# Performance work log

Hardware: AMD Instinct MI355X
Metric: run time of the kernel (lower is better)

The kernel has to match this reference:

```python
import jax, jax.numpy as jnp
import numpy as np

WINDOW_SIZE = (4, 7, 7)  # (t, h, w); N = 4*7*7 = 196


def _relative_position_index(ws):
    t, h, w = ws
    coords = np.stack(np.meshgrid(np.arange(t), np.arange(h), np.arange(w), indexing='ij'))  # (3,t,h,w)
    cf = coords.reshape(3, -1)                      # (3, N)
    rc = (cf[:, :, None] - cf[:, None, :]).transpose(1, 2, 0).astype(np.int64)  # (N, N, 3)
    rc[..., 0] += t - 1
    rc[..., 1] += h - 1
    rc[..., 2] += w - 1
    rc[..., 0] *= (2 * h - 1) * (2 * w - 1)
    rc[..., 1] *= 2 * w - 1
    return rc.sum(-1)                               # (N, N) indices into bias table


def setup_inputs() -> dict:
    key = jax.random.key(0)
    ks = jax.random.split(key, 7)
    B, B_dim, N, C, H = 4, 64, 196, 512, 16
    hd = C // H
    B_ = B * B_dim
    n_bias = (2 * 4 - 1) * (2 * 7 - 1) * (2 * 7 - 1)  # 1183
    return {
        'x': jax.random.normal(ks[0], (B_, N, C), jnp.float32),
        'q_global': jax.random.normal(ks[1], (B, 1, H, N, hd), jnp.float32),
        'kv_w': jax.random.normal(ks[2], (2 * C, C), jnp.float32) * (C ** -0.5),
        'kv_b': jnp.zeros((2 * C,), jnp.float32),
        'proj_w': jax.random.normal(ks[3], (C, C), jnp.float32) * (C ** -0.5),
        'proj_b': jnp.zeros((C,), jnp.float32),
        'bias_table': jax.random.normal(ks[4], (n_bias, H), jnp.float32) * 0.02,
    }


def reference(x, q_global, kv_w, kv_b, proj_w, proj_b, bias_table):
    B_, N, C = x.shape
    B, _, H, _, hd = q_global.shape
    B_dim = B_ // B
    scale = hd ** -0.5

    # kv projection: (B_, N, 2C) -> k, v each (B_, H, N, hd)
    kv = (x @ kv_w.T + kv_b).reshape(B_, N, 2, H, hd).transpose(2, 0, 3, 1, 4)
    keys, values = kv[0], kv[1]

    # global queries repeated across windows: (B,1,H,N,hd) -> (B_, H, N, hd)
    q = jnp.broadcast_to(q_global, (B, B_dim, H, N, hd)).reshape(B_, H, N, hd)
    q = q * scale

    attn = jnp.einsum('bhnd,bhmd->bhnm', q, keys)  # (B_, H, N, N)

    # gathered relative position bias (static index table)
    rpi = jnp.asarray(_relative_position_index(WINDOW_SIZE))  # (N, N)
    bias = bias_table[rpi.reshape(-1)].reshape(N, N, H).transpose(2, 0, 1)  # (H, N, N)
    attn = jax.nn.softmax(attn + bias[None], axis=-1)

    out = jnp.einsum('bhnm,bhmd->bhnd', attn, values)  # (B_, H, N, hd)
    out = out.transpose(0, 2, 1, 3).reshape(B_, N, C)
    return out @ proj_w.T + proj_b
```

## Files before the change

kernel.cpp:

```cpp
#include <hip/hip_runtime.h>
#include <stdint.h>

typedef __attribute__((ext_vector_type(8))) short short8;
typedef __attribute__((ext_vector_type(4))) float f32x4;
typedef __attribute__((ext_vector_type(4))) unsigned short u16x4;

typedef unsigned short ushort_t;

__device__ __forceinline__ unsigned short f2bf(float f) {
    union { float f; uint32_t u; } c; c.f = f;
    uint32_t u = c.u;
    return (unsigned short)((u + 0x7FFFu + ((u >> 16) & 1u)) >> 16);
}

__device__ __forceinline__ f32x4 mfma16(short8 a, short8 b, f32x4 c) {
    return __builtin_amdgcn_mfma_f32_16x16x32_bf16(a, b, c, 0, 0, 0);
}

__device__ __forceinline__ void gl_lds16(const ushort_t* g, ushort_t* l) {
    __builtin_amdgcn_global_load_lds((const __attribute__((address_space(1))) void*)g,
                                     (__attribute__((address_space(3))) void*)l, 16, 0, 0);
}

#define LOG2E 1.4426950408889634f


__global__ __launch_bounds__(256) void cvt_x_k(const float4* __restrict__ in,
                                               u16x4* __restrict__ out, int n4) {
    int i = blockIdx.x * 256 + threadIdx.x;
    if (i < n4) {
        float4 v = in[i];
        u16x4 o;
        o[0] = f2bf(v.x); o[1] = f2bf(v.y); o[2] = f2bf(v.z); o[3] = f2bf(v.w);
        out[i] = o;
    }
}

__global__ __launch_bounds__(256) void cvt_small_k(const float4* __restrict__ kvw,
                                                   const float4* __restrict__ pw,
                                                   const float4* __restrict__ qg,
                                                   u16x4* __restrict__ kvwb,
                                                   u16x4* __restrict__ pwb,
                                                   u16x4* __restrict__ qb) {
    const float qs = 0.17677669529663687f * LOG2E;
    int i = blockIdx.x * 256 + threadIdx.x;
    if (i < 131072) {
        float4 v = kvw[i];
        u16x4 o; o[0]=f2bf(v.x); o[1]=f2bf(v.y); o[2]=f2bf(v.z); o[3]=f2bf(v.w);
        kvwb[i] = o;
    } else if (i < 196608) {
        int j = i - 131072;
        float4 v = pw[j];
        u16x4 o; o[0]=f2bf(v.x); o[1]=f2bf(v.y); o[2]=f2bf(v.z); o[3]=f2bf(v.w);
        pwb[j] = o;
    } else {
        int j = i - 196608;
        float4 v = qg[j];
        u16x4 o; o[0]=f2bf(v.x*qs); o[1]=f2bf(v.y*qs); o[2]=f2bf(v.z*qs); o[3]=f2bf(v.w*qs);
        qb[j] = o;
    }
}

__global__ __launch_bounds__(256) void bias_k(const float* __restrict__ bt,
                                              float* __restrict__ out) {
    int idx = blockIdx.x * 256 + threadIdx.x;
    int h = idx / 43264;
    int rem = idx - h * 43264;
    int i = rem / 208;
    int j = rem - i * 208;
    float v = -1e30f;
    if (i < 196 && j < 196) {
        int t1 = i / 49, r1 = i - t1 * 49, h1 = r1 / 7, w1 = r1 - h1 * 7;
        int t2 = j / 49, r2 = j - t2 * 49, h2 = r2 / 7, w2 = r2 - h2 * 7;
        int bi = (t1 - t2 + 3) * 169 + (h1 - h2 + 6) * 13 + (w1 - w2 + 6);
        v = bt[bi * 16 + h] * LOG2E;
    }
    out[idx] = v;
}

__global__ __launch_bounds__(256) void gemm_kv(const ushort_t* __restrict__ A,
                                               const ushort_t* __restrict__ Bw,
                                               const float* __restrict__ kvb,
                                               ushort_t* __restrict__ Ko,
                                               ushort_t* __restrict__ Vo) {
    __shared__ ushort_t As[128 * 64];
    __shared__ ushort_t Bs[128 * 64];
    const int tid = threadIdx.x;
    const int lane = tid & 63, wave = tid >> 6;
    const int lrow = lane & 15, quad = lane >> 4;
    const int wr = wave >> 1, wc = wave & 1;
    const long arow0 = (long)blockIdx.x * 128;
    const int brow0 = blockIdx.y * 128;

    const int srow = lane >> 3;
    const int scol = ((lane & 7) ^ srow) << 3;
    const int rsw  = (lrow & 7) << 3;

    f32x4 acc[4][4];
#pragma unroll
    for (int i = 0; i < 4; ++i)
#pragma unroll
        for (int j = 0; j < 4; ++j) acc[i][j] = (f32x4){0.f, 0.f, 0.f, 0.f};

    for (int k0 = 0; k0 < 512; k0 += 64) {
#pragma unroll
        for (int t = 0; t < 4; ++t) {
            int rr = wave * 32 + t * 8;
            gl_lds16(&A[(arow0 + rr + srow) * 512 + k0 + scol], &As[rr * 64]);
            gl_lds16(&Bw[(long)(brow0 + rr + srow) * 512 + k0 + scol], &Bs[rr * 64]);
        }
        asm volatile("s_waitcnt vmcnt(0)" ::: "memory");
        __syncthreads();
#pragma unroll
        for (int kk = 0; kk < 64; kk += 32) {
            short8 af[4], bf[4];
#pragma unroll
            for (int i = 0; i < 4; ++i)
                af[i] = *(const short8*)&As[(wr * 64 + i * 16 + lrow) * 64 + ((kk + quad * 8) ^ rsw)];
#pragma unroll
            for (int j = 0; j < 4; ++j)
                bf[j] = *(const short8*)&Bs[(wc * 64 + j * 16 + lrow) * 64 + ((kk + quad * 8) ^ rsw)];
#pragma unroll
            for (int i = 0; i < 4; ++i)
#pragma unroll
                for (int j = 0; j < 4; ++j)
                    acc[i][j] = mfma16(af[i], bf[j], acc[i][j]);
        }
        __syncthreads();
    }
#pragma unroll
    for (int i = 0; i < 4; ++i) {
        int mb = (int)arow0 + wr * 64 + i * 16 + quad * 4;
#pragma unroll
        for (int r = 0; r < 4; ++r) {
            int m = mb + r;
            int b_ = m / 196;
            int n = m - b_ * 196;
#pragma unroll
            for (int j = 0; j < 4; ++j) {
                int cI = brow0 + wc * 64 + j * 16 + lrow;
                float v = acc[i][j][r] + kvb[cI];
                int hh = (cI >> 5) & 15, d = cI & 31;
                ushort_t* dst = (cI >> 9) ? Vo : Ko;
                dst[((((long)b_ << 4) + hh) * 196 + n) * 32 + d] = f2bf(v);
            }
        }
    }
}

__global__ __launch_bounds__(256) void attn_k(const ushort_t* __restrict__ Kb,
                                              const ushort_t* __restrict__ Vb,
                                              const ushort_t* __restrict__ Qb,
                                              const float* __restrict__ biasF,
                                              ushort_t* __restrict__ Ob) {
    const int tid = threadIdx.x, lane = tid & 63, wave = tid >> 6;
    const int lrow = lane & 15, quad = lane >> 4;
    const int bh = blockIdx.x;
    const int b_ = bh >> 4, h = bh & 15;
    const int Bq = b_ >> 6;

    __shared__ ushort_t Vt[32 * 232];
    __shared__ ushort_t Ps[4][16 * 232];

    const long kvoff = (long)bh * 6272;

    for (int i = tid; i < 1024; i += 256) {
        int d = i >> 5, n = 192 + (i & 31);
        Vt[d * 232 + n] = 0;
    }
    __syncthreads();
    for (int i = tid; i < 6272; i += 256) {
        int n = i >> 5, d = i & 31;
        int g = (d >> 3) & 3;
        Vt[d * 232 + (n ^ (g << 3))] = Vb[kvoff + i];
    }
    for (int i = lane; i < 256; i += 64) {
        int r = i >> 4, cp = i & 15;
        Ps[wave][r * 232 + 208 + cp] = 0;
    }
    __syncthreads();

    const float* biasH = biasF + h * 43264;
    const long qbase = (((long)Bq * 16 + h) * 196) * 32;
    const ushort_t* Kh = Kb + kvoff;
    const int vsw0 = ((lrow >> 3) & 1) << 3;
    const int vsw1 = (2 | ((lrow >> 3) & 1)) << 3;

    for (int rt = wave; rt < 13; rt += 4) {
        const int qrow = rt * 16 + lrow;
        const int qr = qrow > 195 ? 195 : qrow;
        short8 qf = *(const short8*)&Qb[qbase + (long)qr * 32 + quad * 8];

        f32x4 s[13];
#pragma unroll
        for (int ct = 0; ct < 13; ++ct) {
            short8 kf = *(const short8*)&Kh[(ct * 16 + lrow) * 32 + quad * 8];
            s[ct] = mfma16(kf, qf, (f32x4){0.f, 0.f, 0.f, 0.f});
        }

        float mx = -3e38f;
        const float* bp = biasH + (long)qrow * 208 + quad * 4;
#pragma unroll
        for (int ct = 0; ct < 13; ++ct) {
            float4 bv = *(const float4*)&bp[ct * 16];
            s[ct][0] += bv.x; s[ct][1] += bv.y; s[ct][2] += bv.z; s[ct][3] += bv.w;
            mx = fmaxf(mx, fmaxf(fmaxf(s[ct][0], s[ct][1]), fmaxf(s[ct][2], s[ct][3])));
        }
        mx = fmaxf(mx, __shfl_xor(mx, 16));
        mx = fmaxf(mx, __shfl_xor(mx, 32));

        float sm = 0.f;
#pragma unroll
        for (int ct = 0; ct < 13; ++ct)
#pragma unroll
            for (int r = 0; r < 4; ++r) {
                float p = exp2f(s[ct][r] - mx);
                s[ct][r] = p;
                sm += p;
            }
        sm += __shfl_xor(sm, 16);
        sm += __shfl_xor(sm, 32);
        const float sminv = 1.0f / sm;

        ushort_t* prow = &Ps[wave][lrow * 232];
#pragma unroll
        for (int ct = 0; ct < 13; ++ct) {
            uint32_t w0, w1;
            asm("v_cvt_pk_bf16_f32 %0, %1, %2" : "=v"(w0) : "v"(s[ct][0]), "v"(s[ct][1]));
            asm("v_cvt_pk_bf16_f32 %0, %1, %2" : "=v"(w1) : "v"(s[ct][2]), "v"(s[ct][3]));
            uint2 w; w.x = w0; w.y = w1;
            *(uint2*)&prow[ct * 16 + quad * 4] = w;
        }
        asm volatile("s_waitcnt lgkmcnt(0)" ::: "memory");

        f32x4 o0 = (f32x4){0.f,0.f,0.f,0.f}, o1 = (f32x4){0.f,0.f,0.f,0.f};
#pragma unroll
        for (int ks = 0; ks < 7; ++ks) {
            short8 pf = *(const short8*)&prow[ks * 32 + quad * 8];
            short8 v0 = *(const short8*)&Vt[lrow * 232 + ((ks * 32 + quad * 8) ^ vsw0)];
            short8 v1 = *(const short8*)&Vt[(16 + lrow) * 232 + ((ks * 32 + quad * 8) ^ vsw1)];
            o0 = mfma16(pf, v0, o0);
            o1 = mfma16(pf, v1, o1);
        }
        const long obase = (long)b_ * 196 * 512 + h * 32;
#pragma unroll
        for (int r = 0; r < 4; ++r) {
            float sv = __shfl(sminv, quad * 4 + r);
            int m = rt * 16 + quad * 4 + r;
            if (m < 196) {
                Ob[obase + (long)m * 512 + lrow]      = f2bf(o0[r] * sv);
                Ob[obase + (long)m * 512 + 16 + lrow] = f2bf(o1[r] * sv);
            }
        }
    }
}

__global__ __launch_bounds__(256) void gemm_proj(const ushort_t* __restrict__ A,
                                                 const ushort_t* __restrict__ Bw,
                                                 const float* __restrict__ pb,
                                                 float* __restrict__ out) {
    __shared__ ushort_t As[128 * 64];
    __shared__ ushort_t Bs[128 * 64];
    const int tid = threadIdx.x;
    const int lane = tid & 63, wave = tid >> 6;
    const int lrow = lane & 15, quad = lane >> 4;
    const int wr = wave >> 1, wc = wave & 1;
    const long arow0 = (long)blockIdx.x * 128;
    const int brow0 = blockIdx.y * 128;

    const int srow = lane >> 3;
    const int scol = ((lane & 7) ^ srow) << 3;
    const int rsw  = (lrow & 7) << 3;

    f32x4 acc[4][4];
#pragma unroll
    for (int i = 0; i < 4; ++i)
#pragma unroll
        for (int j = 0; j < 4; ++j) acc[i][j] = (f32x4){0.f, 0.f, 0.f, 0.f};

    for (int k0 = 0; k0 < 512; k0 += 64) {
#pragma unroll
        for (int t = 0; t < 4; ++t) {
            int rr = wave * 32 + t * 8;
            gl_lds16(&A[(arow0 + rr + srow) * 512 + k0 + scol], &As[rr * 64]);
            gl_lds16(&Bw[(long)(brow0 + rr + srow) * 512 + k0 + scol], &Bs[rr * 64]);
        }
        asm volatile("s_waitcnt vmcnt(0)" ::: "memory");
        __syncthreads();
#pragma unroll
        for (int kk = 0; kk < 64; kk += 32) {
            short8 af[4], bf[4];
#pragma unroll
            for (int i = 0; i < 4; ++i)
                af[i] = *(const short8*)&As[(wr * 64 + i * 16 + lrow) * 64 + ((kk + quad * 8) ^ rsw)];
#pragma unroll
            for (int j = 0; j < 4; ++j)
                bf[j] = *(const short8*)&Bs[(wc * 64 + j * 16 + lrow) * 64 + ((kk + quad * 8) ^ rsw)];
#pragma unroll
            for (int i = 0; i < 4; ++i)
#pragma unroll
                for (int j = 0; j < 4; ++j)
                    acc[i][j] = mfma16(af[i], bf[j], acc[i][j]);
        }
        __syncthreads();
    }
#pragma unroll
    for (int i = 0; i < 4; ++i) {
        long mb = arow0 + wr * 64 + i * 16 + quad * 4;
#pragma unroll
        for (int r = 0; r < 4; ++r) {
            long m = mb + r;
#pragma unroll
            for (int j = 0; j < 4; ++j) {
                int cI = brow0 + wc * 64 + j * 16 + lrow;
                out[m * 512 + cI] = acc[i][j][r] + pb[cI];
            }
        }
    }
}


extern "C" void kernel_launch(void* const* d_in, const int* in_sizes, int n_in,
                              void* d_out, int out_size, void* d_ws, size_t ws_size,
                              hipStream_t stream) {
    const float* x   = (const float*)d_in[0];
    const float* qg  = (const float*)d_in[1];
    const float* kvw = (const float*)d_in[2];
    const float* kvb = (const float*)d_in[3];
    const float* pw  = (const float*)d_in[4];
    const float* pb  = (const float*)d_in[5];
    const float* bt  = (const float*)d_in[6];
    float* out = (float*)d_out;

    char* ws = (char*)d_ws;
    ushort_t* xb    = (ushort_t*)(ws);
    ushort_t* kbuf  = (ushort_t*)(ws + 51380224);
    ushort_t* vbuf  = (ushort_t*)(ws + 102760448);
    ushort_t* kvwb  = (ushort_t*)(ws + 154140672);
    ushort_t* pwb   = (ushort_t*)(ws + 155189248);
    ushort_t* qb    = (ushort_t*)(ws + 155713536);
    float*    biasF = (float*)   (ws + 156516352);
    ushort_t* obuf  = xb;

    cvt_x_k<<<25088, 256, 0, stream>>>((const float4*)x, (u16x4*)xb, 6422528);
    cvt_small_k<<<1160, 256, 0, stream>>>((const float4*)kvw, (const float4*)pw,
                                          (const float4*)qg,
                                          (u16x4*)kvwb, (u16x4*)pwb, (u16x4*)qb);
    bias_k<<<2704, 256, 0, stream>>>(bt, biasF);
    gemm_kv<<<dim3(392, 8), 256, 0, stream>>>(xb, kvwb, kvb, kbuf, vbuf);
    attn_k<<<4096, 256, 0, stream>>>(kbuf, vbuf, qb, biasF, obuf);
    gemm_proj<<<dim3(392, 4), 256, 0, stream>>>(obuf, pwb, pb, out);
}
```

Measured before the change: 446.0 us.

## Store V transposed from the KV GEMM and read it directly in attention

The KV projection epilogue now writes V in a transposed, padded layout (head-dim major, 200-wide token rows), packing four consecutive tokens per store. A small kernel zeroes the four padding columns of each row. The attention kernel no longer stages and transposes V through shared memory with scalar stores and barriers; it loads the B fragments for the P·V MMA straight from global memory. This removes the per-block LDS transpose and its barriers. In exchange, each wave rereads V from cache and the K and V output stores in the GEMM epilogue become more scattered.

```diff
diff --git a/kernel.cpp b/kernel.cpp
--- a/kernel.cpp
+++ b/kernel.cpp
@@ -61,6 +61,12 @@
     }
 }
 
+__global__ __launch_bounds__(256) void zeroT_k(ushort_t* __restrict__ vt) {
+    int i = blockIdx.x * 256 + threadIdx.x;
+    u16x4 z = (u16x4){0, 0, 0, 0};
+    *(u16x4*)&vt[(long)i * 200 + 196] = z;
+}
+
 __global__ __launch_bounds__(256) void bias_k(const float* __restrict__ bt,
                                               float* __restrict__ out) {
     int idx = blockIdx.x * 256 + threadIdx.x;
@@ -131,25 +137,31 @@
 #pragma unroll
     for (int i = 0; i < 4; ++i) {
         int mb = (int)arow0 + wr * 64 + i * 16 + quad * 4;
-#pragma unroll
-        for (int r = 0; r < 4; ++r) {
-            int m = mb + r;
-            int b_ = m / 196;
-            int n = m - b_ * 196;
-#pragma unroll
-            for (int j = 0; j < 4; ++j) {
-                int cI = brow0 + wc * 64 + j * 16 + lrow;
-                float v = acc[i][j][r] + kvb[cI];
-                int hh = (cI >> 5) & 15, d = cI & 31;
-                ushort_t* dst = (cI >> 9) ? Vo : Ko;
-                dst[((((long)b_ << 4) + hh) * 196 + n) * 32 + d] = f2bf(v);
+        int b_ = mb / 196;
+        int n = mb - b_ * 196;
+#pragma unroll
+        for (int j = 0; j < 4; ++j) {
+            int cI = brow0 + wc * 64 + j * 16 + lrow;
+            float bias = kvb[cI];
+            int hh = (cI >> 5) & 15, d = cI & 31;
+            if (cI < 512) {
+                long base = ((((long)b_ << 4) + hh) * 196 + n) * 32 + d;
+#pragma unroll
+                for (int r = 0; r < 4; ++r)
+                    Ko[base + (long)r * 32] = f2bf(acc[i][j][r] + bias);
+            } else {
+                long base = ((((long)b_ << 4) + hh) * 32 + d) * 200 + n;
+                u16x4 o;
+#pragma unroll
+                for (int r = 0; r < 4; ++r) o[r] = f2bf(acc[i][j][r] + bias);
+                *(u16x4*)&Vo[base] = o;
             }
         }
     }
 }
 
 __global__ __launch_bounds__(256) void attn_k(const ushort_t* __restrict__ Kb,
-                                              const ushort_t* __restrict__ Vb,
+                                              const ushort_t* __restrict__ VtG,
                                               const ushort_t* __restrict__ Qb,
                                               const float* __restrict__ biasF,
                                               ushort_t* __restrict__ Ob) {
@@ -159,32 +171,17 @@
     const int b_ = bh >> 4, h = bh & 15;
     const int Bq = b_ >> 6;
 
-    __shared__ ushort_t Vt[32 * 232];
     __shared__ ushort_t Ps[4][16 * 232];
 
-    const long kvoff = (long)bh * 6272;
-
-    for (int i = tid; i < 1024; i += 256) {
-        int d = i >> 5, n = 192 + (i & 31);
-        Vt[d * 232 + n] = 0;
-    }
-    __syncthreads();
-    for (int i = tid; i < 6272; i += 256) {
-        int n = i >> 5, d = i & 31;
-        int g = (d >> 3) & 3;
-        Vt[d * 232 + (n ^ (g << 3))] = Vb[kvoff + i];
-    }
     for (int i = lane; i < 256; i += 64) {
         int r = i >> 4, cp = i & 15;
         Ps[wave][r * 232 + 208 + cp] = 0;
     }
-    __syncthreads();
 
     const float* biasH = biasF + h * 43264;
     const long qbase = (((long)Bq * 16 + h) * 196) * 32;
-    const ushort_t* Kh = Kb + kvoff;
-    const int vsw0 = ((lrow >> 3) & 1) << 3;
-    const int vsw1 = (2 | ((lrow >> 3) & 1)) << 3;
+    const ushort_t* Kh = Kb + (long)bh * 6272;
+    const ushort_t* Vh = VtG + (long)bh * 6400;
 
     for (int rt = wave; rt < 13; rt += 4) {
         const int qrow = rt * 16 + lrow;
@@ -236,9 +233,11 @@
         f32x4 o0 = (f32x4){0.f,0.f,0.f,0.f}, o1 = (f32x4){0.f,0.f,0.f,0.f};
 #pragma unroll
         for (int ks = 0; ks < 7; ++ks) {
-            short8 pf = *(const short8*)&prow[ks * 32 + quad * 8];
-            short8 v0 = *(const short8*)&Vt[lrow * 232 + ((ks * 32 + quad * 8) ^ vsw0)];
-            short8 v1 = *(const short8*)&Vt[(16 + lrow) * 232 + ((ks * 32 + quad * 8) ^ vsw1)];
+            int c = ks * 32 + quad * 8;
+            int vc = (c < 200) ? c : 0;
+            short8 pf = *(const short8*)&prow[c];
+            short8 v0 = *(const short8*)&Vh[lrow * 200 + vc];
+            short8 v1 = *(const short8*)&Vh[(16 + lrow) * 200 + vc];
             o0 = mfma16(pf, v0, o0);
             o1 = mfma16(pf, v1, o1);
         }
@@ -335,19 +334,20 @@
     char* ws = (char*)d_ws;
     ushort_t* xb    = (ushort_t*)(ws);
     ushort_t* kbuf  = (ushort_t*)(ws + 51380224);
-    ushort_t* vbuf  = (ushort_t*)(ws + 102760448);
-    ushort_t* kvwb  = (ushort_t*)(ws + 154140672);
-    ushort_t* pwb   = (ushort_t*)(ws + 155189248);
-    ushort_t* qb    = (ushort_t*)(ws + 155713536);
-    float*    biasF = (float*)   (ws + 156516352);
+    ushort_t* vbufT = (ushort_t*)(ws + 102760448);
+    ushort_t* kvwb  = (ushort_t*)(ws + 155189248);
+    ushort_t* pwb   = (ushort_t*)(ws + 156237824);
+    ushort_t* qb    = (ushort_t*)(ws + 156762112);
+    float*    biasF = (float*)   (ws + 157564928);
     ushort_t* obuf  = xb;
 
     cvt_x_k<<<25088, 256, 0, stream>>>((const float4*)x, (u16x4*)xb, 6422528);
     cvt_small_k<<<1160, 256, 0, stream>>>((const float4*)kvw, (const float4*)pw,
                                           (const float4*)qg,
                                           (u16x4*)kvwb, (u16x4*)pwb, (u16x4*)qb);
+    zeroT_k<<<512, 256, 0, stream>>>(vbufT);
     bias_k<<<2704, 256, 0, stream>>>(bt, biasF);
-    gemm_kv<<<dim3(392, 8), 256, 0, stream>>>(xb, kvwb, kvb, kbuf, vbuf);
-    attn_k<<<4096, 256, 0, stream>>>(kbuf, vbuf, qb, biasF, obuf);
+    gemm_kv<<<dim3(392, 8), 256, 0, stream>>>(xb, kvwb, kvb, kbuf, vbufT);
+    attn_k<<<4096, 256, 0, stream>>>(kbuf, vbufT, qb, biasF, obuf);
     gemm_proj<<<dim3(392, 4), 256, 0, stream>>>(obuf, pwb, pb, out);
 }
```

Result: slower. 463.9 us (+4.0%).
